# Kernel optimization log

Measured on AMD Instinct MI355X. Metric: run time of the kernel, lower is better.

The kernel has to match this reference:

```python
import jax, jax.numpy as jnp
import numpy as np


def setup_inputs() -> dict:
    key = jax.random.key(0)
    k1, k2 = jax.random.split(key)
    B, C, H, W = 64, 64, 32, 32
    ROWS, COLS, O, KH, KW = 28, 28, 128, 5, 5
    x = jax.random.normal(k1, (B, C, H, W), dtype=jnp.float32)
    weight = jax.random.normal(k2, (ROWS, COLS, O, C, KH, KW), dtype=jnp.float32) * 0.05
    return {"x": x, "weight": weight}


def reference(x, weight):
    # Locally-connected conv (unshared weights), stride 1, no padding.
    # output[b,o,i,j] = sum_{c,u,v} x[b,c,i+u,j+v] * weight[i,j,o,c,u,v]
    rows, cols, O, C, kh, kw = weight.shape
    # patches: [B, C, kh, kw, rows, cols] built from kh*kw shifted views (small fixed loop)
    patches = jnp.stack(
        [jnp.stack([x[:, :, u:u + rows, v:v + cols] for v in range(kw)], axis=2)
         for u in range(kh)], axis=2)
    return jnp.einsum('bcuvij,ijocuv->boij', patches, weight)
```

## Files before the change

kernel.cpp:

```cpp
#include <hip/hip_runtime.h>


typedef __attribute__((ext_vector_type(8))) short bf16x8;
typedef __attribute__((ext_vector_type(4))) float f32x4;

__device__ __forceinline__ unsigned short f2bf(float f) {
    unsigned int u = __float_as_uint(f);
    u = (u + 0x7fffu + ((u >> 16) & 1u)) >> 16;
    return (unsigned short)u;
}

__global__ __launch_bounds__(256, 3) void lconv_mfma(
    const float* __restrict__ x,
    const float* __restrict__ wgt,
    float* __restrict__ out)
{
    constexpr int K   = 1600;
    constexpr int KC  = 64;
    constexpr int LDK = KC + 8;
    constexpr int O   = 128;
    constexpr int POS = 784;

    __shared__ unsigned short As[64][LDK];

    const int bx = blockIdx.x;
    const int g = (bx & 7) * 98 + (bx >> 3);
    const int i = g / 28;
    const int j = g - i * 28;

    const int t    = threadIdx.x;
    const int lane = t & 63;
    const int wv   = t >> 6;
    const int l15  = lane & 15;
    const int quad = lane >> 4;

    const float* xbase = x + i * 32 + j;
    const int sb = t >> 2;
    const int sk = (t & 3) * 16;
    const float* xrow = xbase + sb * 65536;

    const float* wpos = wgt + (size_t)g * (size_t)(O * K);

    f32x4 acc[4][2];
#pragma unroll
    for (int mt = 0; mt < 4; ++mt)
#pragma unroll
        for (int nt = 0; nt < 2; ++nt)
            acc[mt][nt] = (f32x4)0.f;

    for (int kb = 0; kb < K; kb += KC) {
        unsigned int pk[8];
#pragma unroll
        for (int e = 0; e < 16; e += 2) {
            int k0 = kb + sk + e;
            int c0 = k0 / 25, r0 = k0 - 25 * c0;
            int u0 = r0 / 5,  v0 = r0 - 5 * u0;
            int k1 = k0 + 1;
            int c1 = k1 / 25, r1 = k1 - 25 * c1;
            int u1 = r1 / 5,  v1 = r1 - 5 * u1;
            float f0 = xrow[c0 * 1024 + u0 * 32 + v0];
            float f1 = xrow[c1 * 1024 + u1 * 32 + v1];
            pk[e >> 1] = (unsigned int)f2bf(f0) | ((unsigned int)f2bf(f1) << 16);
        }
        {
            uint4 q0 = make_uint4(pk[0], pk[1], pk[2], pk[3]);
            uint4 q1 = make_uint4(pk[4], pk[5], pk[6], pk[7]);
            *(uint4*)&As[sb][sk]     = q0;
            *(uint4*)&As[sb][sk + 8] = q1;
        }
        __syncthreads();

#pragma unroll
        for (int kk = 0; kk < 2; ++kk) {
            bf16x8 bfr[2];
#pragma unroll
            for (int nt = 0; nt < 2; ++nt) {
                const int o = wv * 32 + nt * 16 + l15;
                const float* wp = wpos + (size_t)o * K + (kb + kk * 32 + quad * 8);
                f32x4 w0 = *(const f32x4*)wp;
                f32x4 w1 = *(const f32x4*)(wp + 4);
                bf16x8 bv;
                bv[0] = (short)f2bf(w0[0]); bv[1] = (short)f2bf(w0[1]);
                bv[2] = (short)f2bf(w0[2]); bv[3] = (short)f2bf(w0[3]);
                bv[4] = (short)f2bf(w1[0]); bv[5] = (short)f2bf(w1[1]);
                bv[6] = (short)f2bf(w1[2]); bv[7] = (short)f2bf(w1[3]);
                bfr[nt] = bv;
            }
#pragma unroll
            for (int mt = 0; mt < 4; ++mt) {
                bf16x8 av = *(const bf16x8*)&As[mt * 16 + l15][kk * 32 + quad * 8];
#pragma unroll
                for (int nt = 0; nt < 2; ++nt)
                    acc[mt][nt] = __builtin_amdgcn_mfma_f32_16x16x32_bf16(
                        av, bfr[nt], acc[mt][nt], 0, 0, 0);
            }
        }
        __syncthreads();
    }

#pragma unroll
    for (int mt = 0; mt < 4; ++mt) {
#pragma unroll
        for (int nt = 0; nt < 2; ++nt) {
            const int o = wv * 32 + nt * 16 + l15;
#pragma unroll
            for (int r = 0; r < 4; ++r) {
                const int b = mt * 16 + quad * 4 + r;
                out[((size_t)b * O + o) * POS + g] = acc[mt][nt][r];
            }
        }
    }
}

extern "C" void kernel_launch(void* const* d_in, const int* in_sizes, int n_in,
                              void* d_out, int out_size, void* d_ws, size_t ws_size,
                              hipStream_t stream) {
    const float* x   = (const float*)d_in[0];
    const float* wgt = (const float*)d_in[1];
    float* out       = (float*)d_out;
    lconv_mfma<<<784, 256, 0, stream>>>(x, wgt, out);
}
```

Before: 1.190 ms.

## Pre-pack bf16 im2col patches, split K across two blocks with async LDS staging

```diff
diff --git a/kernel.cpp b/kernel.cpp
--- a/kernel.cpp
+++ b/kernel.cpp
@@ -3,11 +3,137 @@
 
 typedef __attribute__((ext_vector_type(8))) short bf16x8;
 typedef __attribute__((ext_vector_type(4))) float f32x4;
-
-__device__ __forceinline__ unsigned short f2bf(float f) {
-    unsigned int u = __float_as_uint(f);
+typedef unsigned int u32;
+typedef unsigned short u16;
+
+__device__ __forceinline__ u16 f2bf(float f) {
+    u32 u = __float_as_uint(f);
     u = (u + 0x7fffu + ((u >> 16) & 1u)) >> 16;
-    return (unsigned short)u;
+    return (u16)u;
+}
+
+__global__ __launch_bounds__(256) void pack_x(const float* __restrict__ x,
+                                              u16* __restrict__ P) {
+    const int b  = blockIdx.x >> 3;
+    const int cg = blockIdx.x & 7;
+    const int t  = threadIdx.x;
+    __shared__ u16 Xs[8 * 1024];
+
+    const float* xb = x + b * 65536 + cg * 8192;
+#pragma unroll
+    for (int r = 0; r < 8; ++r) {
+        int off = r * 1024 + t * 4;
+        f32x4 v = *(const f32x4*)(xb + off);
+        *(u32*)&Xs[off]     = (u32)f2bf(v[0]) | ((u32)f2bf(v[1]) << 16);
+        *(u32*)&Xs[off + 2] = (u32)f2bf(v[2]) | ((u32)f2bf(v[3]) << 16);
+    }
+    __syncthreads();
+
+    u32* Pd = (u32*)P;
+    for (int idx = t; idx < 78400; idx += 256) {
+        int g   = idx / 100;
+        int rem = idx - g * 100;
+        int i = g / 28;
+        int j = g - i * 28;
+        int e0 = rem * 2;
+        int c0 = e0 / 25, r0 = e0 - c0 * 25, u0 = r0 / 5, v0 = r0 - u0 * 5;
+        int e1 = e0 + 1;
+        int c1 = e1 / 25, r1 = e1 - c1 * 25, u1 = r1 / 5, v1 = r1 - u1 * 5;
+        u16 a0 = Xs[c0 * 1024 + (i + u0) * 32 + (j + v0)];
+        u16 a1 = Xs[c1 * 1024 + (i + u1) * 32 + (j + v1)];
+        int kg = cg * 200 + e0;
+        int cb = kg / 160;
+        int kc = kg - cb * 160;
+        Pd[((g * 10 + cb) * 64 + b) * 80 + (kc >> 1)] = (u32)a0 | ((u32)a1 << 16);
+    }
+}
+
+__device__ __forceinline__ void glds16(const void* g, void* l) {
+    __builtin_amdgcn_global_load_lds(
+        (const __attribute__((address_space(1))) u32*)g,
+        (__attribute__((address_space(3))) u32*)l, 16, 0, 0);
+}
+
+__global__ __launch_bounds__(256, 4) void lconv_main(const float* __restrict__ wgt,
+                                                     const u16* __restrict__ P,
+                                                     float* __restrict__ out) {
+    constexpr int KC = 160;
+    __shared__ u16 As[2][64 * KC];
+
+    const int bx = blockIdx.x;
+    const int s  = bx & 1;
+    const int bq = bx >> 1;
+    const int g  = (bq & 7) * 98 + (bq >> 3);
+
+    const int t = threadIdx.x, lane = t & 63, wv = t >> 6;
+    const int l15 = lane & 15, quad = lane >> 4;
+
+    const u16*   Pg = P + (size_t)g * 102400 + (size_t)s * 5 * 10240;
+    const float* wg = wgt + (size_t)g * 204800 + (size_t)s * 800;
+
+    f32x4 acc[4][2];
+#pragma unroll
+    for (int mt = 0; mt < 4; ++mt)
+#pragma unroll
+        for (int nt = 0; nt < 2; ++nt)
+            acc[mt][nt] = (f32x4)0.f;
+
+    auto stage = [&](int cb, int buf) {
+        const char* src = (const char*)(Pg + cb * 10240);
+        char* dst = (char*)&As[buf][0];
+#pragma unroll
+        for (int r = 0; r < 5; ++r) {
+            int off = wv * 1024 + r * 4096;
+            glds16(src + off + lane * 16, dst + off);
+        }
+    };
+
+    stage(0, 0);
+    __syncthreads();
+
+    for (int cb = 0; cb < 5; ++cb) {
+        if (cb < 4) stage(cb + 1, (cb + 1) & 1);
+        const u16*   A  = As[cb & 1];
+        const float* wc = wg + cb * 160;
+#pragma unroll
+        for (int ks = 0; ks < 5; ++ks) {
+            bf16x8 bfr[2];
+#pragma unroll
+            for (int nt = 0; nt < 2; ++nt) {
+                const int o = wv * 32 + nt * 16 + l15;
+                const float* wp = wc + (size_t)o * 1600 + ks * 32 + quad * 8;
+                f32x4 w0 = __builtin_nontemporal_load((const f32x4*)wp);
+                f32x4 w1 = __builtin_nontemporal_load((const f32x4*)wp + 1);
+                bf16x8 bv;
+                bv[0] = (short)f2bf(w0[0]); bv[1] = (short)f2bf(w0[1]);
+                bv[2] = (short)f2bf(w0[2]); bv[3] = (short)f2bf(w0[3]);
+                bv[4] = (short)f2bf(w1[0]); bv[5] = (short)f2bf(w1[1]);
+                bv[6] = (short)f2bf(w1[2]); bv[7] = (short)f2bf(w1[3]);
+                bfr[nt] = bv;
+            }
+#pragma unroll
+            for (int mt = 0; mt < 4; ++mt) {
+                bf16x8 av = *(const bf16x8*)&A[(mt * 16 + l15) * KC + ks * 32 + quad * 8];
+#pragma unroll
+                for (int nt = 0; nt < 2; ++nt)
+                    acc[mt][nt] = __builtin_amdgcn_mfma_f32_16x16x32_bf16(
+                        av, bfr[nt], acc[mt][nt], 0, 0, 0);
+            }
+        }
+        if (cb < 4) __syncthreads();
+    }
+
+#pragma unroll
+    for (int mt = 0; mt < 4; ++mt)
+#pragma unroll
+        for (int nt = 0; nt < 2; ++nt) {
+            const int o = wv * 32 + nt * 16 + l15;
+#pragma unroll
+            for (int r = 0; r < 4; ++r) {
+                const int b = mt * 16 + quad * 4 + r;
+                atomicAdd(&out[((size_t)b * 128 + o) * 784 + g], acc[mt][nt][r]);
+            }
+        }
 }
 
 __global__ __launch_bounds__(256, 3) void lconv_mfma(
@@ -15,61 +141,37 @@
     const float* __restrict__ wgt,
     float* __restrict__ out)
 {
-    constexpr int K   = 1600;
-    constexpr int KC  = 64;
-    constexpr int LDK = KC + 8;
-    constexpr int O   = 128;
-    constexpr int POS = 784;
-
-    __shared__ unsigned short As[64][LDK];
-
+    constexpr int K = 1600, KC = 64, LDK = KC + 8, O = 128, POS = 784;
+    __shared__ u16 As[64][LDK];
     const int bx = blockIdx.x;
     const int g = (bx & 7) * 98 + (bx >> 3);
-    const int i = g / 28;
-    const int j = g - i * 28;
-
-    const int t    = threadIdx.x;
-    const int lane = t & 63;
-    const int wv   = t >> 6;
-    const int l15  = lane & 15;
-    const int quad = lane >> 4;
-
+    const int i = g / 28, j = g - i * 28;
+    const int t = threadIdx.x, lane = t & 63, wv = t >> 6;
+    const int l15 = lane & 15, quad = lane >> 4;
     const float* xbase = x + i * 32 + j;
-    const int sb = t >> 2;
-    const int sk = (t & 3) * 16;
+    const int sb = t >> 2, sk = (t & 3) * 16;
     const float* xrow = xbase + sb * 65536;
-
     const float* wpos = wgt + (size_t)g * (size_t)(O * K);
-
     f32x4 acc[4][2];
 #pragma unroll
     for (int mt = 0; mt < 4; ++mt)
 #pragma unroll
-        for (int nt = 0; nt < 2; ++nt)
-            acc[mt][nt] = (f32x4)0.f;
-
+        for (int nt = 0; nt < 2; ++nt) acc[mt][nt] = (f32x4)0.f;
     for (int kb = 0; kb < K; kb += KC) {
-        unsigned int pk[8];
+        u32 pk[8];
 #pragma unroll
         for (int e = 0; e < 16; e += 2) {
             int k0 = kb + sk + e;
-            int c0 = k0 / 25, r0 = k0 - 25 * c0;
-            int u0 = r0 / 5,  v0 = r0 - 5 * u0;
+            int c0 = k0 / 25, r0 = k0 - 25 * c0, u0 = r0 / 5, v0 = r0 - 5 * u0;
             int k1 = k0 + 1;
-            int c1 = k1 / 25, r1 = k1 - 25 * c1;
-            int u1 = r1 / 5,  v1 = r1 - 5 * u1;
+            int c1 = k1 / 25, r1 = k1 - 25 * c1, u1 = r1 / 5, v1 = r1 - 5 * u1;
             float f0 = xrow[c0 * 1024 + u0 * 32 + v0];
             float f1 = xrow[c1 * 1024 + u1 * 32 + v1];
-            pk[e >> 1] = (unsigned int)f2bf(f0) | ((unsigned int)f2bf(f1) << 16);
-        }
-        {
-            uint4 q0 = make_uint4(pk[0], pk[1], pk[2], pk[3]);
-            uint4 q1 = make_uint4(pk[4], pk[5], pk[6], pk[7]);
-            *(uint4*)&As[sb][sk]     = q0;
-            *(uint4*)&As[sb][sk + 8] = q1;
-        }
+            pk[e >> 1] = (u32)f2bf(f0) | ((u32)f2bf(f1) << 16);
+        }
+        *(uint4*)&As[sb][sk]     = make_uint4(pk[0], pk[1], pk[2], pk[3]);
+        *(uint4*)&As[sb][sk + 8] = make_uint4(pk[4], pk[5], pk[6], pk[7]);
         __syncthreads();
-
 #pragma unroll
         for (int kk = 0; kk < 2; ++kk) {
             bf16x8 bfr[2];
@@ -97,9 +199,8 @@
         }
         __syncthreads();
     }
-
-#pragma unroll
-    for (int mt = 0; mt < 4; ++mt) {
+#pragma unroll
+    for (int mt = 0; mt < 4; ++mt)
 #pragma unroll
         for (int nt = 0; nt < 2; ++nt) {
             const int o = wv * 32 + nt * 16 + l15;
@@ -109,7 +210,6 @@
                 out[((size_t)b * O + o) * POS + g] = acc[mt][nt][r];
             }
         }
-    }
 }
 
 extern "C" void kernel_launch(void* const* d_in, const int* in_sizes, int n_in,
@@ -118,5 +218,12 @@
     const float* x   = (const float*)d_in[0];
     const float* wgt = (const float*)d_in[1];
     float* out       = (float*)d_out;
-    lconv_mfma<<<784, 256, 0, stream>>>(x, wgt, out);
-}
+    const size_t PBYTES = 784ull * 10 * 64 * 160 * 2;
+    if (ws_size >= PBYTES) {
+        hipMemsetAsync(d_out, 0, (size_t)out_size * sizeof(float), stream);
+        pack_x<<<512, 256, 0, stream>>>(x, (u16*)d_ws);
+        lconv_main<<<1568, 256, 0, stream>>>(wgt, (const u16*)d_ws, out);
+    } else {
+        lconv_mfma<<<784, 256, 0, stream>>>(x, wgt, out);
+    }
+}
```

Result: slower. 1.478 ms (+24.2%).
